# Optimization experiments

Hardware: AMD Instinct MI355X
Metric: run time of the kernel (lower is better)

Reference implementation:

```python
import jax, jax.numpy as jnp
import numpy as np


def setup_inputs() -> dict:
    key = jax.random.key(0)
    k1, k2, k3 = jax.random.split(key, 3)
    B, N, D = 64, 2048, 1024
    output = jax.random.normal(k1, (B, 1, D), dtype=jnp.float32)
    context = jax.random.normal(k2, (B, N, D), dtype=jnp.float32)
    # nn.Linear(2*dim, dim): weight [dim, 2*dim], bias [dim]
    W_out = jax.random.normal(k3, (D, 2 * D), dtype=jnp.float32) * (1.0 / np.sqrt(2 * D))
    b_out = jnp.zeros((D,), dtype=jnp.float32)
    return {"output": output, "context": context, "W_out": W_out, "b_out": b_out}


def reference(output, context, W_out, b_out):
    B, q, D = output.shape  # q == 1
    N = context.shape[1]
    # scores: (B, q, N) = output @ context^T
    attn = jnp.einsum('bqd,bnd->bqn', output, context)
    attn = jax.nn.softmax(attn, axis=-1)
    # mix: (B, q, D)
    mix = jnp.einsum('bqn,bnd->bqd', attn, context)
    combined = jnp.concatenate([mix, output], axis=-1)  # (B, q, 2D)
    out = jnp.tanh(jnp.einsum('bqe,de->bqd', combined, W_out) + b_out)
    return (out, attn)
```

## Files before the change

### kernel.cpp

```cpp
#include <hip/hip_runtime.h>
#include <cmath>

#define BATCH 64
#define NCTX 2048
#define DIM 1024
#define CHUNKS 16
#define ROWS_PER_CHUNK (NCTX / CHUNKS)
#define ROWS_PER_WAVE (ROWS_PER_CHUNK / 4)

typedef float f4_t __attribute__((ext_vector_type(4)));

__global__ __launch_bounds__(256) void attn_phase1(
    const float* __restrict__ q,
    const float* __restrict__ ctx,
    float* __restrict__ scores,
    float* __restrict__ part_m,
    float* __restrict__ part_l,
    float* __restrict__ part_o)
{
    const int blk  = blockIdx.x;
    const int b    = blk / CHUNKS;
    const int c    = blk % CHUNKS;
    const int tid  = threadIdx.x;
    const int wave = tid >> 6;
    const int lane = tid & 63;

    f4_t qf[4];
    const float* qb = q + (size_t)b * DIM;
    #pragma unroll
    for (int j = 0; j < 4; ++j)
        qf[j] = *reinterpret_cast<const f4_t*>(qb + lane * 4 + 256 * j);

    float m = -INFINITY, l = 0.f;
    f4_t o[4];
    #pragma unroll
    for (int j = 0; j < 4; ++j) o[j] = (f4_t)(0.f);

    const int row0 = c * ROWS_PER_CHUNK + wave * ROWS_PER_WAVE;
    const float* cb = ctx + (size_t)b * NCTX * DIM;
    float* sc = scores + (size_t)b * NCTX;

    for (int i = 0; i < ROWS_PER_WAVE; i += 4) {
        f4_t cf[4][4];
        #pragma unroll
        for (int r = 0; r < 4; ++r) {
            const float* cr = cb + (size_t)(row0 + i + r) * DIM + lane * 4;
            #pragma unroll
            for (int j = 0; j < 4; ++j)
                cf[r][j] = __builtin_nontemporal_load(
                    reinterpret_cast<const f4_t*>(cr + 256 * j));
        }

        float s[4];
        #pragma unroll
        for (int r = 0; r < 4; ++r) {
            float d0 = qf[0].x * cf[r][0].x + qf[0].y * cf[r][0].y
                     + qf[0].z * cf[r][0].z + qf[0].w * cf[r][0].w;
            float d1 = qf[1].x * cf[r][1].x + qf[1].y * cf[r][1].y
                     + qf[1].z * cf[r][1].z + qf[1].w * cf[r][1].w;
            float d2 = qf[2].x * cf[r][2].x + qf[2].y * cf[r][2].y
                     + qf[2].z * cf[r][2].z + qf[2].w * cf[r][2].w;
            float d3 = qf[3].x * cf[r][3].x + qf[3].y * cf[r][3].y
                     + qf[3].z * cf[r][3].z + qf[3].w * cf[r][3].w;
            s[r] = (d0 + d1) + (d2 + d3);
        }

        #pragma unroll
        for (int off = 32; off >= 1; off >>= 1) {
            s[0] += __shfl_xor(s[0], off, 64);
            s[1] += __shfl_xor(s[1], off, 64);
            s[2] += __shfl_xor(s[2], off, 64);
            s[3] += __shfl_xor(s[3], off, 64);
        }

        {
            float sv = (lane == 1) ? s[1] : (lane == 2) ? s[2]
                     : (lane == 3) ? s[3] : s[0];
            if (lane < 4) sc[row0 + i + lane] = sv;
        }

        const float mx = fmaxf(fmaxf(s[0], s[1]), fmaxf(s[2], s[3]));
        const float m_new = fmaxf(m, mx);
        if (m_new > m) {
            const float a = __expf(m - m_new);
            l *= a;
            #pragma unroll
            for (int j = 0; j < 4; ++j) o[j] *= a;
            m = m_new;
        }
        const float p0 = __expf(s[0] - m);
        const float p1 = __expf(s[1] - m);
        const float p2 = __expf(s[2] - m);
        const float p3 = __expf(s[3] - m);
        l += (p0 + p1) + (p2 + p3);
        #pragma unroll
        for (int j = 0; j < 4; ++j) {
            o[j].x += p0 * cf[0][j].x + p1 * cf[1][j].x
                    + p2 * cf[2][j].x + p3 * cf[3][j].x;
            o[j].y += p0 * cf[0][j].y + p1 * cf[1][j].y
                    + p2 * cf[2][j].y + p3 * cf[3][j].y;
            o[j].z += p0 * cf[0][j].z + p1 * cf[1][j].z
                    + p2 * cf[2][j].z + p3 * cf[3][j].z;
            o[j].w += p0 * cf[0][j].w + p1 * cf[1][j].w
                    + p2 * cf[2][j].w + p3 * cf[3][j].w;
        }
    }

    __shared__ float wm[4], wl[4];
    __shared__ float o_lds[4 * DIM];
    if (lane == 0) { wm[wave] = m; wl[wave] = l; }
    __syncthreads();

    const float Mb = fmaxf(fmaxf(wm[0], wm[1]), fmaxf(wm[2], wm[3]));
    float Lb = 0.f;
    #pragma unroll
    for (int w = 0; w < 4; ++w) Lb += wl[w] * __expf(wm[w] - Mb);

    const float aw = __expf(m - Mb);
    #pragma unroll
    for (int j = 0; j < 4; ++j) {
        f4_t t = o[j] * aw;
        *reinterpret_cast<f4_t*>(&o_lds[wave * DIM + lane * 4 + 256 * j]) = t;
    }
    __syncthreads();

    {
        const int e = tid * 4;
        f4_t s0 = *reinterpret_cast<const f4_t*>(&o_lds[0 * DIM + e]);
        f4_t s1 = *reinterpret_cast<const f4_t*>(&o_lds[1 * DIM + e]);
        f4_t s2 = *reinterpret_cast<const f4_t*>(&o_lds[2 * DIM + e]);
        f4_t s3 = *reinterpret_cast<const f4_t*>(&o_lds[3 * DIM + e]);
        f4_t r = (s0 + s1) + (s2 + s3);
        *reinterpret_cast<f4_t*>(&part_o[((size_t)b * CHUNKS + c) * DIM + e]) = r;
    }
    if (tid == 0) {
        part_m[b * CHUNKS + c] = Mb;
        part_l[b * CHUNKS + c] = Lb;
    }
}

__global__ __launch_bounds__(256) void attn_phase2(
    const float* __restrict__ scores,
    const float* __restrict__ part_m,
    const float* __restrict__ part_l,
    const float* __restrict__ part_o,
    float* __restrict__ mix,
    float* __restrict__ attn_out)
{
    const int b    = blockIdx.x >> 2;
    const int part = blockIdx.x & 3;
    const int tid  = threadIdx.x;

    float M = -INFINITY;
    #pragma unroll
    for (int i = 0; i < CHUNKS; ++i) M = fmaxf(M, part_m[b * CHUNKS + i]);

    float w[CHUNKS];
    float L = 0.f;
    #pragma unroll
    for (int i = 0; i < CHUNKS; ++i) {
        w[i] = __expf(part_m[b * CHUNKS + i] - M);
        L += part_l[b * CHUNKS + i] * w[i];
    }
    const float invL = 1.f / L;

    {
        const int e = part * 256 + tid;
        float acc = 0.f;
        #pragma unroll
        for (int i = 0; i < CHUNKS; ++i)
            acc += part_o[((size_t)b * CHUNKS + i) * DIM + e] * w[i];
        mix[(size_t)b * DIM + e] = acc * invL;
    }

    #pragma unroll
    for (int t = 0; t < 2; ++t) {
        const int n = part * 512 + t * 256 + tid;
        attn_out[(size_t)b * NCTX + n] =
            __expf(scores[(size_t)b * NCTX + n] - M) * invL;
    }
}

#define BT 4
#define DT 32
__global__ __launch_bounds__(256) void attn_phase3(
    const float* __restrict__ mix,
    const float* __restrict__ q,
    const float* __restrict__ W,
    const float* __restrict__ bias,
    float* __restrict__ out)
{
    const int d_chunk = blockIdx.x % (DIM / DT);
    const int b_chunk = blockIdx.x / (DIM / DT);
    const int d0 = d_chunk * DT;
    const int b0 = b_chunk * BT;
    const int tid  = threadIdx.x;
    const int wave = tid >> 6;
    const int lane = tid & 63;

    __shared__ float comb[BT * 2 * DIM];
    for (int i = tid; i < BT * 2 * DIM; i += 256) {
        const int bl = i >> 11;
        const int e  = i & 2047;
        comb[i] = (e < DIM) ? mix[(size_t)(b0 + bl) * DIM + e]
                            : q[(size_t)(b0 + bl) * DIM + (e - DIM)];
    }
    __syncthreads();

    const int d_base = d0 + wave * (DT / 4);
    #pragma unroll
    for (int g = 0; g < 2; ++g) {
        const int dg = d_base + g * 4;
        float acc[4][BT];
        #pragma unroll
        for (int di = 0; di < 4; ++di)
            #pragma unroll
            for (int bl = 0; bl < BT; ++bl) acc[di][bl] = 0.f;

        for (int kk = 0; kk < 2 * DIM; kk += 256) {
            f4_t wv[4];
            #pragma unroll
            for (int di = 0; di < 4; ++di)
                wv[di] = *reinterpret_cast<const f4_t*>(
                    W + (size_t)(dg + di) * (2 * DIM) + kk + lane * 4);
            #pragma unroll
            for (int bl = 0; bl < BT; ++bl) {
                f4_t cv = *reinterpret_cast<const f4_t*>(
                    &comb[bl * 2 * DIM + kk + lane * 4]);
                #pragma unroll
                for (int di = 0; di < 4; ++di) {
                    acc[di][bl] += wv[di].x * cv.x;
                    acc[di][bl] += wv[di].y * cv.y;
                    acc[di][bl] += wv[di].z * cv.z;
                    acc[di][bl] += wv[di].w * cv.w;
                }
            }
        }

        float myval = 0.f;
        #pragma unroll
        for (int di = 0; di < 4; ++di) {
            #pragma unroll
            for (int bl = 0; bl < BT; ++bl) {
                float v = acc[di][bl];
                #pragma unroll
                for (int off = 32; off >= 1; off >>= 1)
                    v += __shfl_xor(v, off, 64);
                if (lane == di * BT + bl) myval = v;
            }
        }
        if (lane < 16) {
            const int di = lane >> 2;
            const int bl = lane & 3;
            const int d  = dg + di;
            out[(size_t)(b0 + bl) * DIM + d] = tanhf(myval + bias[d]);
        }
    }
}

extern "C" void kernel_launch(void* const* d_in, const int* in_sizes, int n_in,
                              void* d_out, int out_size, void* d_ws, size_t ws_size,
                              hipStream_t stream) {
    const float* q    = (const float*)d_in[0];
    const float* ctx  = (const float*)d_in[1];
    const float* W    = (const float*)d_in[2];
    const float* bias = (const float*)d_in[3];

    float* out_main = (float*)d_out;
    float* attn_out = (float*)d_out + (size_t)BATCH * DIM;

    float* ws      = (float*)d_ws;
    float* scores  = ws;
    float* part_m  = scores + (size_t)BATCH * NCTX;
    float* part_l  = part_m + BATCH * CHUNKS;
    float* part_o  = part_l + BATCH * CHUNKS;
    float* mix     = part_o + (size_t)BATCH * CHUNKS * DIM;

    attn_phase1<<<BATCH * CHUNKS, 256, 0, stream>>>(q, ctx, scores,
                                                    part_m, part_l, part_o);
    attn_phase2<<<BATCH * 4, 256, 0, stream>>>(scores, part_m, part_l, part_o,
                                               mix, attn_out);
    attn_phase3<<<(DIM / DT) * (BATCH / BT), 256, 0, stream>>>(mix, q, W, bias,
                                                               out_main);
}
```

Measured before the change: 673.6 us.

## Double-buffer context row loads in phase1 and retile phase3 GEMV

Phase1 now software-pipelines context reads with two register buffers. The loads for the next 4 rows are issued before the current 4 rows are processed, and the 8-step loop is fully unrolled. Phase3 is retiled to 8 batches by 16 outputs per block, with each wave handling 4 outputs in one pass. It also uses vectorized float4 staging into LDS and doubles LDS use to 64KB. The goal is to hide HBM latency in the bandwidth-bound context stream and to reuse each W load across more batches, at the cost of higher register pressure and lower occupancy.

```diff
diff --git a/kernel.cpp b/kernel.cpp
--- a/kernel.cpp
+++ b/kernel.cpp
@@ -40,8 +40,7 @@
     const float* cb = ctx + (size_t)b * NCTX * DIM;
     float* sc = scores + (size_t)b * NCTX;
 
-    for (int i = 0; i < ROWS_PER_WAVE; i += 4) {
-        f4_t cf[4][4];
+    auto loadrows = [&](f4_t (&cf)[4][4], int i) {
         #pragma unroll
         for (int r = 0; r < 4; ++r) {
             const float* cr = cb + (size_t)(row0 + i + r) * DIM + lane * 4;
@@ -50,7 +49,9 @@
                 cf[r][j] = __builtin_nontemporal_load(
                     reinterpret_cast<const f4_t*>(cr + 256 * j));
         }
-
+    };
+
+    auto process = [&](f4_t (&cf)[4][4], int i) {
         float s[4];
         #pragma unroll
         for (int r = 0; r < 4; ++r) {
@@ -103,6 +104,19 @@
                     + p2 * cf[2][j].z + p3 * cf[3][j].z;
             o[j].w += p0 * cf[0][j].w + p1 * cf[1][j].w
                     + p2 * cf[2][j].w + p3 * cf[3][j].w;
+        }
+    };
+
+    f4_t cfA[4][4], cfB[4][4];
+    loadrows(cfA, 0);
+    #pragma unroll
+    for (int ii = 0; ii < 8; ++ii) {
+        if (ii & 1) {
+            if (ii < 7) loadrows(cfA, (ii + 1) * 4);
+            process(cfB, ii * 4);
+        } else {
+            if (ii < 7) loadrows(cfB, (ii + 1) * 4);
+            process(cfA, ii * 4);
         }
     }
 
@@ -181,8 +195,8 @@
     }
 }
 
-#define BT 4
-#define DT 32
+#define BT3 8
+#define DT3 16
 __global__ __launch_bounds__(256) void attn_phase3(
     const float* __restrict__ mix,
     const float* __restrict__ q,
@@ -190,71 +204,74 @@
     const float* __restrict__ bias,
     float* __restrict__ out)
 {
-    const int d_chunk = blockIdx.x % (DIM / DT);
-    const int b_chunk = blockIdx.x / (DIM / DT);
-    const int d0 = d_chunk * DT;
-    const int b0 = b_chunk * BT;
+    const int d_chunk = blockIdx.x % (DIM / DT3);
+    const int b_chunk = blockIdx.x / (DIM / DT3);
+    const int d0 = d_chunk * DT3;
+    const int b0 = b_chunk * BT3;
     const int tid  = threadIdx.x;
     const int wave = tid >> 6;
     const int lane = tid & 63;
 
-    __shared__ float comb[BT * 2 * DIM];
-    for (int i = tid; i < BT * 2 * DIM; i += 256) {
-        const int bl = i >> 11;
-        const int e  = i & 2047;
-        comb[i] = (e < DIM) ? mix[(size_t)(b0 + bl) * DIM + e]
-                            : q[(size_t)(b0 + bl) * DIM + (e - DIM)];
+    __shared__ float comb[BT3 * 2 * DIM];
+
+    {
+        const f4_t* mix4 = reinterpret_cast<const f4_t*>(mix);
+        const f4_t* q4   = reinterpret_cast<const f4_t*>(q);
+        f4_t* comb4      = reinterpret_cast<f4_t*>(comb);
+        for (int i = tid; i < BT3 * 2 * DIM / 4; i += 256) {
+            const int bl = i >> 9;
+            const int e4 = i & 511;
+            comb4[i] = (e4 < 256) ? mix4[(size_t)(b0 + bl) * 256 + e4]
+                                  : q4[(size_t)(b0 + bl) * 256 + (e4 - 256)];
+        }
     }
     __syncthreads();
 
-    const int d_base = d0 + wave * (DT / 4);
-    #pragma unroll
-    for (int g = 0; g < 2; ++g) {
-        const int dg = d_base + g * 4;
-        float acc[4][BT];
+    const int dg = d0 + wave * 4;
+    float acc[4][BT3];
+    #pragma unroll
+    for (int di = 0; di < 4; ++di)
+        #pragma unroll
+        for (int bl = 0; bl < BT3; ++bl) acc[di][bl] = 0.f;
+
+    #pragma unroll 2
+    for (int kk = 0; kk < 2 * DIM; kk += 256) {
+        f4_t wv[4];
         #pragma unroll
         for (int di = 0; di < 4; ++di)
+            wv[di] = *reinterpret_cast<const f4_t*>(
+                W + (size_t)(dg + di) * (2 * DIM) + kk + lane * 4);
+        #pragma unroll
+        for (int bl = 0; bl < BT3; ++bl) {
+            f4_t cv = *reinterpret_cast<const f4_t*>(
+                &comb[bl * 2 * DIM + kk + lane * 4]);
             #pragma unroll
-            for (int bl = 0; bl < BT; ++bl) acc[di][bl] = 0.f;
-
-        for (int kk = 0; kk < 2 * DIM; kk += 256) {
-            f4_t wv[4];
+            for (int di = 0; di < 4; ++di) {
+                acc[di][bl] += wv[di].x * cv.x;
+                acc[di][bl] += wv[di].y * cv.y;
+                acc[di][bl] += wv[di].z * cv.z;
+                acc[di][bl] += wv[di].w * cv.w;
+            }
+        }
+    }
+
+    float myval = 0.f;
+    #pragma unroll
+    for (int di = 0; di < 4; ++di) {
+        #pragma unroll
+        for (int bl = 0; bl < BT3; ++bl) {
+            float v = acc[di][bl];
             #pragma unroll
-            for (int di = 0; di < 4; ++di)
-                wv[di] = *reinterpret_cast<const f4_t*>(
-                    W + (size_t)(dg + di) * (2 * DIM) + kk + lane * 4);
-            #pragma unroll
-            for (int bl = 0; bl < BT; ++bl) {
-                f4_t cv = *reinterpret_cast<const f4_t*>(
-                    &comb[bl * 2 * DIM + kk + lane * 4]);
-                #pragma unroll
-                for (int di = 0; di < 4; ++di) {
-                    acc[di][bl] += wv[di].x * cv.x;
-                    acc[di][bl] += wv[di].y * cv.y;
-                    acc[di][bl] += wv[di].z * cv.z;
-                    acc[di][bl] += wv[di].w * cv.w;
-                }
-            }
-        }
-
-        float myval = 0.f;
-        #pragma unroll
-        for (int di = 0; di < 4; ++di) {
-            #pragma unroll
-            for (int bl = 0; bl < BT; ++bl) {
-                float v = acc[di][bl];
-                #pragma unroll
-                for (int off = 32; off >= 1; off >>= 1)
-                    v += __shfl_xor(v, off, 64);
-                if (lane == di * BT + bl) myval = v;
-            }
-        }
-        if (lane < 16) {
-            const int di = lane >> 2;
-            const int bl = lane & 3;
-            const int d  = dg + di;
-            out[(size_t)(b0 + bl) * DIM + d] = tanhf(myval + bias[d]);
-        }
+            for (int off = 32; off >= 1; off >>= 1)
+                v += __shfl_xor(v, off, 64);
+            if (lane == di * BT3 + bl) myval = v;
+        }
+    }
+    if (lane < 32) {
+        const int di = lane >> 3;
+        const int bl = lane & 7;
+        const int d  = dg + di;
+        out[(size_t)(b0 + bl) * DIM + d] = tanhf(myval + bias[d]);
     }
 }
 
@@ -280,6 +297,6 @@
                                                     part_m, part_l, part_o);
     attn_phase2<<<BATCH * 4, 256, 0, stream>>>(scores, part_m, part_l, part_o,
                                                mix, attn_out);
-    attn_phase3<<<(DIM / DT) * (BATCH / BT), 256, 0, stream>>>(mix, q, W, bias,
-                                                               out_main);
+    attn_phase3<<<(DIM / DT3) * (BATCH / BT3), 256, 0, stream>>>(mix, q, W, bias,
+                                                                 out_main);
 }
```

Measured after the change: 672.8 us. No clear change (-0.1%).
